# Performance work log

Hardware: AMD Instinct MI355X
Metric: run time of the kernel (lower is better)

## Reference

```python
import jax, jax.numpy as jnp
import numpy as np

# ---- static config (matches init_kwargs / input_specs) ----
MODEL_CONTEXT_LEN = 4096
BLOCK_SIZE = 16
NUM_Q_HEADS = 32
NUM_KV_HEADS = 8
HEAD_DIM = 128
ROPE_BASE = 10000.0
B = 8
NUM_PAST = 4613                                   # context_len - 1, same for all seqs
END_BNUM = NUM_PAST // BLOCK_SIZE                 # 288
REM = NUM_PAST % BLOCK_SIZE                       # 5
START_BNUM = (NUM_PAST - MODEL_CONTEXT_LEN) // BLOCK_SIZE + 2  # 34
CUR_POS = MODEL_CONTEXT_LEN - 1                   # 4095 (capped decode position)
BLOCKS_PER_SEQ = END_BNUM + 1                     # 289
NUM_BLOCKS = B * BLOCKS_PER_SEQ                   # 2312


def rope(pos, x):
    """NeoX-style rotary. pos: [T] int; x: [..., T, H, D]."""
    half = HEAD_DIM // 2
    inv = 1.0 / (ROPE_BASE ** (jnp.arange(half, dtype=jnp.float32) / half))
    freqs = pos.astype(jnp.float32)[:, None] * inv        # [T, half]
    cos = jnp.cos(freqs)[:, None, :]                      # [T, 1, half]
    sin = jnp.sin(freqs)[:, None, :]
    x1, x2 = jnp.split(x, 2, axis=-1)
    return jnp.concatenate([x1 * cos - x2 * sin, x2 * cos + x1 * sin], axis=-1)


def setup_inputs() -> dict:
    key = jax.random.key(0)
    ks = jax.random.split(key, 7)
    q = jax.random.normal(ks[0], (B, NUM_Q_HEADS * HEAD_DIM), jnp.float32)
    k = jax.random.normal(ks[1], (B, NUM_KV_HEADS * HEAD_DIM), jnp.float32)
    v = jax.random.normal(ks[2], (B, NUM_KV_HEADS * HEAD_DIM), jnp.float32)
    positions = jnp.full((B,), NUM_PAST, dtype=jnp.int32)
    context_lens = jnp.full((B,), NUM_PAST + 1, dtype=jnp.int32)
    # distinct physical blocks per sequence (paged layout)
    block_tables = jnp.arange(NUM_BLOCKS, dtype=jnp.int32).reshape(B, BLOCKS_PER_SEQ)
    # cache stores UN-rotated keys (module writes k_original); layout [nblk, bs, Hk, D]
    key_cache = jax.random.normal(ks[3], (NUM_BLOCKS, BLOCK_SIZE, NUM_KV_HEADS, HEAD_DIM), jnp.float32) * 0.5
    value_cache = jax.random.normal(ks[4], (NUM_BLOCKS, BLOCK_SIZE, NUM_KV_HEADS, HEAD_DIM), jnp.float32) * 0.5
    W_o = jax.random.normal(ks[5], (NUM_Q_HEADS * HEAD_DIM, NUM_Q_HEADS * HEAD_DIM), jnp.float32) * 0.02
    return {"q": q, "k": k, "v": v, "positions": positions, "context_lens": context_lens,
            "block_tables": block_tables, "key_cache": key_cache, "value_cache": value_cache, "W_o": W_o}


def reference(q, k, v, positions, context_lens, block_tables, key_cache, value_cache, W_o):
    # Decode path of StreamingAttentionSink, context > model_context_len:
    # gather sink block + sliding-window blocks, re-apply rotary at shifted
    # positions, attend with q/k roped at capped position, project output.
    # positions for re-roped past keys: sink tokens 0..bs-1, window tokens
    # 2*bs-1-rem .. model_context_len-2 (matches the torch code's pos arange).
    pos_sink = np.arange(BLOCK_SIZE)
    pos_win = np.arange(2 * BLOCK_SIZE - 1 - REM, MODEL_CONTEXT_LEN - 1)
    POS = jnp.asarray(np.concatenate([pos_sink, pos_win]), dtype=jnp.int32)  # [4085]

    qh = q.reshape(B, NUM_Q_HEADS, HEAD_DIM)
    kh = k.reshape(B, NUM_KV_HEADS, HEAD_DIM)
    vh = v.reshape(B, NUM_KV_HEADS, HEAD_DIM)

    # phys_bnums = [block_table[0]] + block_table[start:end]  -> [B, 255]
    phys = jnp.concatenate([block_tables[:, :1], block_tables[:, START_BNUM:END_BNUM]], axis=1)
    full_k = key_cache[phys].reshape(B, -1, NUM_KV_HEADS, HEAD_DIM)       # [B, 4080, Hk, D]
    rem_k = key_cache[block_tables[:, END_BNUM], :REM]                     # [B, 5, Hk, D]
    past_k = jnp.concatenate([full_k, rem_k], axis=1)                      # [B, 4085, Hk, D]
    full_v = value_cache[phys].reshape(B, -1, NUM_KV_HEADS, HEAD_DIM)
    rem_v = value_cache[block_tables[:, END_BNUM], :REM]
    past_v = jnp.concatenate([full_v, rem_v], axis=1)

    past_k = rope(POS, past_k)  # re-apply rotary to shifted sink/window keys

    cur = jnp.array([CUR_POS], dtype=jnp.int32)
    q_rot = rope(cur, qh[:, None, :, :])[:, 0]   # [B, H, D] at capped position
    k_rot = rope(cur, kh[:, None, :, :])[:, 0]   # [B, Hk, D]

    keys = jnp.concatenate([past_k, k_rot[:, None]], axis=1)   # [B, 4086, Hk, D]
    vals = jnp.concatenate([past_v, vh[:, None]], axis=1)

    # GQA attention (group = 4 q-heads per kv-head)
    G = NUM_Q_HEADS // NUM_KV_HEADS
    qg = q_rot.reshape(B, NUM_KV_HEADS, G, HEAD_DIM)
    scale = 1.0 / np.sqrt(HEAD_DIM).astype(np.float32)
    scores = jnp.einsum('bhgd,bthd->bhgt', qg, keys) * scale
    probs = jax.nn.softmax(scores, axis=-1)
    attn = jnp.einsum('bhgt,bthd->bhgd', probs, vals).reshape(B, NUM_Q_HEADS * HEAD_DIM)
    return attn @ W_o
```

## Files before the change

kernel.cpp:

```cpp
#include <hip/hip_runtime.h>
#include <math.h>

#define NB 8
#define NQH 32
#define NKVH 8
#define HD 128
#define GQ 4
#define T_TOT 4086
#define SPLITS 16
#define TCHUNK 256
#define TILE 32
#define PAD 132
#define BPS 289
#define LOG2_10K_OVER_64 0.2076205059304601f
#define SCALE 0.08838834764831843f

#define PART_ATTN_OFF 0
#define PART_ATTN_SZ  (64 * GQ * SPLITS * PAD)
#define ATTN_OFF      (PART_ATTN_OFF + PART_ATTN_SZ)
#define ATTN_SZ       (NB * 4096)
#define PART_GEMM_OFF (ATTN_OFF + ATTN_SZ)
#define PART_GEMM_SZ  (16 * 32768)

__global__ __launch_bounds__(256) void attn_partial_kernel(
    const float* __restrict__ q, const float* __restrict__ k, const float* __restrict__ v,
    const int* __restrict__ bt, const float* __restrict__ kc, const float* __restrict__ vc,
    float* __restrict__ part)
{
    __shared__ float kt[TILE][PAD];
    __shared__ float vt[TILE][PAD];
    __shared__ float qs[GQ][HD];
    __shared__ float sc[GQ][TILE];
    __shared__ float inv_s[64];
    __shared__ int   ptile[TILE];

    const int tid  = threadIdx.x;
    const int bh   = blockIdx.x;
    const int s    = blockIdx.y;
    const int b    = bh >> 3, h = bh & 7;
    const int lane = tid & 63, wave = tid >> 6;

    if (tid < 64) inv_s[tid] = exp2f(-(float)tid * LOG2_10K_OVER_64);
    __syncthreads();

    const float* qp = q + (size_t)b * (NQH * HD) + (size_t)h * (GQ * HD);
    for (int e = tid; e < GQ * HD; e += 256) {
        int g = e >> 7, d = e & 127, j = d & 63;
        float freq = 4095.0f * inv_s[j];
        float sn, cs; sincosf(freq, &sn, &cs);
        float x1 = qp[g * HD + j], x2 = qp[g * HD + j + 64];
        qs[g][d] = (d < 64) ? (x1 * cs - x2 * sn) : (x2 * cs + x1 * sn);
    }

    float m_run = -INFINITY, l_run = 0.0f, acc_lo = 0.0f, acc_hi = 0.0f;
    const int t0 = s * TCHUNK;
    const int* btb = bt + b * BPS;

    for (int tb = 0; tb < TCHUNK; tb += TILE) {
        __syncthreads();

        for (int e = tid; e < TILE * 32; e += 256) {
            int row = e >> 5, c4 = (e & 31) << 2;
            int tg = t0 + tb + row;
            if (tg <= T_TOT - 1) {
                const float *ksrc, *vsrc; int pos;
                if (tg == T_TOT - 1) {
                    ksrc = k + (size_t)(b * NKVH + h) * HD;
                    vsrc = v + (size_t)(b * NKVH + h) * HD;
                    pos = 4095;
                } else {
                    int bti, rr;
                    if (tg < 16)        { bti = 0;              rr = tg;        pos = tg;      }
                    else if (tg < 4080) { bti = 33 + (tg >> 4); rr = tg & 15;   pos = tg + 10; }
                    else                { bti = 288;            rr = tg - 4080; pos = tg + 10; }
                    int blk = btb[bti];
                    size_t off = (((size_t)blk * 16 + rr) * NKVH + h) * HD;
                    ksrc = kc + off; vsrc = vc + off;
                }
                float4 kk = *(const float4*)(ksrc + c4);
                float4 vv = *(const float4*)(vsrc + c4);
                *(float4*)&kt[row][c4] = kk;
                *(float4*)&vt[row][c4] = vv;
                if ((e & 31) == 0) ptile[row] = pos;
            } else {
                float4 z = {0.f, 0.f, 0.f, 0.f};
                *(float4*)&kt[row][c4] = z;
                *(float4*)&vt[row][c4] = z;
                if ((e & 31) == 0) ptile[row] = 0;
            }
        }
        __syncthreads();

        for (int e = tid; e < TILE * 64; e += 256) {
            int row = e >> 6, j = e & 63;
            float freq = (float)ptile[row] * inv_s[j];
            float sn, cs; sincosf(freq, &sn, &cs);
            float x1 = kt[row][j], x2 = kt[row][j + 64];
            kt[row][j]      = x1 * cs - x2 * sn;
            kt[row][j + 64] = x2 * cs + x1 * sn;
        }
        __syncthreads();

        if (tid < 128) {
            int t = tid & 31, g = tid >> 5;
            int tg = t0 + tb + t;
            float dot = 0.f;
            #pragma unroll
            for (int d4 = 0; d4 < 32; ++d4) {
                float4 kk = *(const float4*)&kt[t][d4 << 2];
                float4 qq = *(const float4*)&qs[g][d4 << 2];
                dot += kk.x * qq.x + kk.y * qq.y + kk.z * qq.z + kk.w * qq.w;
            }
            sc[g][t] = (tg <= T_TOT - 1) ? dot * SCALE : -INFINITY;
        }
        __syncthreads();

        {
            int g = wave;
            int tl = lane & 31;
            float sv = sc[g][tl];
            float mx = sv;
            #pragma unroll
            for (int off = 16; off; off >>= 1) mx = fmaxf(mx, __shfl_xor(mx, off));
            float m_new = fmaxf(m_run, mx);
            float alpha = expf(m_run - m_new);
            float p = expf(sv - m_new);
            float ps = p;
            #pragma unroll
            for (int off = 16; off; off >>= 1) ps += __shfl_xor(ps, off);
            l_run = l_run * alpha + ps;
            m_run = m_new;
            acc_lo *= alpha; acc_hi *= alpha;
            if (lane < 32) sc[g][tl] = p;
            #pragma unroll 8
            for (int t = 0; t < TILE; ++t) {
                float pv = sc[g][t];
                acc_lo += pv * vt[t][lane];
                acc_hi += pv * vt[t][lane + 64];
            }
        }
    }

    float* pp = part + ((size_t)(bh * GQ + wave) * SPLITS + s) * PAD;
    pp[lane] = acc_lo;
    pp[lane + 64] = acc_hi;
    if (lane == 0) { pp[128] = m_run; pp[129] = l_run; }
}

__global__ __launch_bounds__(256) void attn_reduce_kernel(
    const float* __restrict__ part, float* __restrict__ attn)
{
    int bh = blockIdx.x;
    int tid = threadIdx.x;
    int g = tid >> 6, lane = tid & 63;
    const float* pg = part + (size_t)(bh * GQ + g) * SPLITS * PAD;
    float mstar = -INFINITY;
    #pragma unroll
    for (int s = 0; s < SPLITS; ++s) mstar = fmaxf(mstar, pg[s * PAD + 128]);
    float accl = 0.f, acch = 0.f, l = 0.f;
    #pragma unroll
    for (int s = 0; s < SPLITS; ++s) {
        float w = expf(pg[s * PAD + 128] - mstar);
        l    += pg[s * PAD + 129] * w;
        accl += w * pg[s * PAD + lane];
        acch += w * pg[s * PAD + lane + 64];
    }
    int b = bh >> 3, h = bh & 7;
    float inv_l = 1.0f / l;
    size_t base = (size_t)b * 4096 + (size_t)(h * GQ + g) * 128;
    attn[base + lane]      = accl * inv_l;
    attn[base + lane + 64] = acch * inv_l;
}

__global__ __launch_bounds__(256) void gemm_partial_kernel(
    const float* __restrict__ attn, const float* __restrict__ Wo,
    float* __restrict__ part)
{
    __shared__ float a_s[NB][256];
    int tid = threadIdx.x;
    int jt = blockIdx.x & 15, is = blockIdx.x >> 4;
    int i0 = is * 256;
    int c  = jt * 256 + tid;
    for (int e = tid; e < NB * 256; e += 256) {
        int bb = e >> 8, i = e & 255;
        a_s[bb][i] = attn[(size_t)bb * 4096 + i0 + i];
    }
    __syncthreads();
    float acc[NB] = {0.f, 0.f, 0.f, 0.f, 0.f, 0.f, 0.f, 0.f};
    #pragma unroll 4
    for (int i = 0; i < 256; ++i) {
        float w = Wo[(size_t)(i0 + i) * 4096 + c];
        #pragma unroll
        for (int bb = 0; bb < NB; ++bb) acc[bb] += a_s[bb][i] * w;
    }
    for (int bb = 0; bb < NB; ++bb)
        part[(size_t)is * 32768 + (size_t)bb * 4096 + c] = acc[bb];
}

__global__ __launch_bounds__(256) void gemm_reduce_kernel(
    const float* __restrict__ part, float* __restrict__ out)
{
    int idx = blockIdx.x * 256 + threadIdx.x;
    float4 sum = {0.f, 0.f, 0.f, 0.f};
    #pragma unroll
    for (int s = 0; s < 16; ++s) {
        float4 p = *(const float4*)(part + (size_t)s * 32768 + (size_t)idx * 4);
        sum.x += p.x; sum.y += p.y; sum.z += p.z; sum.w += p.w;
    }
    *(float4*)(out + (size_t)idx * 4) = sum;
}

extern "C" void kernel_launch(void* const* d_in, const int* in_sizes, int n_in,
                              void* d_out, int out_size, void* d_ws, size_t ws_size,
                              hipStream_t stream) {
    const float* q  = (const float*)d_in[0];
    const float* k  = (const float*)d_in[1];
    const float* v  = (const float*)d_in[2];
    const int*   bt = (const int*)d_in[5];
    const float* kc = (const float*)d_in[6];
    const float* vc = (const float*)d_in[7];
    const float* Wo = (const float*)d_in[8];
    float* out = (float*)d_out;
    float* ws  = (float*)d_ws;

    float* part_attn = ws + PART_ATTN_OFF;
    float* attn      = ws + ATTN_OFF;
    float* part_gemm = ws + PART_GEMM_OFF;

    attn_partial_kernel<<<dim3(64, SPLITS), 256, 0, stream>>>(q, k, v, bt, kc, vc, part_attn);
    attn_reduce_kernel<<<64, 256, 0, stream>>>(part_attn, attn);
    gemm_partial_kernel<<<256, 256, 0, stream>>>(attn, Wo, part_gemm);
    gemm_reduce_kernel<<<32, 256, 0, stream>>>(part_gemm, out);
}
```

Before: 397.0 us.

## Precompute RoPE cos/sin table, fuse key rotation into load, split GEMM over more blocks

Adds a kernel that precomputes a 4096x128 cos/sin table in workspace, so the attention kernel no longer calls sincosf per key element. Key rotation is now done in registers as the key is loaded, which removes a shared-memory pass and one barrier per tile. The output GEMM grid grows from 256 to 1024 blocks, each covering 64 columns with a 4-way wave split over the reduction dimension and a shared-memory reduction, to raise parallelism. The cost is an extra launch plus table writes and reads, and the gemm partials now reuse the table's workspace region.

```diff
diff --git a/kernel.cpp b/kernel.cpp
--- a/kernel.cpp
+++ b/kernel.cpp
@@ -15,24 +15,33 @@
 #define LOG2_10K_OVER_64 0.2076205059304601f
 #define SCALE 0.08838834764831843f
 
-#define PART_ATTN_OFF 0
+#define TAB_OFF       0
+#define TAB_SZ        (4096 * 128)
+#define PART_GEMM_OFF 0
+#define PART_ATTN_OFF TAB_SZ
 #define PART_ATTN_SZ  (64 * GQ * SPLITS * PAD)
 #define ATTN_OFF      (PART_ATTN_OFF + PART_ATTN_SZ)
-#define ATTN_SZ       (NB * 4096)
-#define PART_GEMM_OFF (ATTN_OFF + ATTN_SZ)
-#define PART_GEMM_SZ  (16 * 32768)
+
+__global__ __launch_bounds__(256) void rope_table_kernel(float* __restrict__ tab)
+{
+    int idx = blockIdx.x * 256 + threadIdx.x;
+    int pos = idx >> 6, j = idx & 63;
+    float inv = exp2f(-(float)j * LOG2_10K_OVER_64);
+    float freq = (float)pos * inv;
+    float sn, cs; sincosf(freq, &sn, &cs);
+    tab[pos * 128 + j]      = cs;
+    tab[pos * 128 + 64 + j] = sn;
+}
 
 __global__ __launch_bounds__(256) void attn_partial_kernel(
     const float* __restrict__ q, const float* __restrict__ k, const float* __restrict__ v,
     const int* __restrict__ bt, const float* __restrict__ kc, const float* __restrict__ vc,
-    float* __restrict__ part)
+    const float* __restrict__ tab, float* __restrict__ part)
 {
     __shared__ float kt[TILE][PAD];
     __shared__ float vt[TILE][PAD];
     __shared__ float qs[GQ][HD];
     __shared__ float sc[GQ][TILE];
-    __shared__ float inv_s[64];
-    __shared__ int   ptile[TILE];
 
     const int tid  = threadIdx.x;
     const int bh   = blockIdx.x;
@@ -40,14 +49,11 @@
     const int b    = bh >> 3, h = bh & 7;
     const int lane = tid & 63, wave = tid >> 6;
 
-    if (tid < 64) inv_s[tid] = exp2f(-(float)tid * LOG2_10K_OVER_64);
-    __syncthreads();
-
     const float* qp = q + (size_t)b * (NQH * HD) + (size_t)h * (GQ * HD);
+    const float* trow = tab + 4095 * 128;
     for (int e = tid; e < GQ * HD; e += 256) {
         int g = e >> 7, d = e & 127, j = d & 63;
-        float freq = 4095.0f * inv_s[j];
-        float sn, cs; sincosf(freq, &sn, &cs);
+        float cs = trow[j], sn = trow[64 + j];
         float x1 = qp[g * HD + j], x2 = qp[g * HD + j + 64];
         qs[g][d] = (d < 64) ? (x1 * cs - x2 * sn) : (x2 * cs + x1 * sn);
     }
@@ -59,14 +65,13 @@
     for (int tb = 0; tb < TCHUNK; tb += TILE) {
         __syncthreads();
 
-        for (int e = tid; e < TILE * 32; e += 256) {
-            int row = e >> 5, c4 = (e & 31) << 2;
+        for (int e = tid; e < TILE * 16; e += 256) {
+            int row = e >> 4, c4 = (e & 15) << 2;
             int tg = t0 + tb + row;
             if (tg <= T_TOT - 1) {
-                const float *ksrc, *vsrc; int pos;
+                const float* ksrc; int pos;
                 if (tg == T_TOT - 1) {
                     ksrc = k + (size_t)(b * NKVH + h) * HD;
-                    vsrc = v + (size_t)(b * NKVH + h) * HD;
                     pos = 4095;
                 } else {
                     int bti, rr;
@@ -74,30 +79,45 @@
                     else if (tg < 4080) { bti = 33 + (tg >> 4); rr = tg & 15;   pos = tg + 10; }
                     else                { bti = 288;            rr = tg - 4080; pos = tg + 10; }
                     int blk = btb[bti];
-                    size_t off = (((size_t)blk * 16 + rr) * NKVH + h) * HD;
-                    ksrc = kc + off; vsrc = vc + off;
+                    ksrc = kc + (((size_t)blk * 16 + rr) * NKVH + h) * HD;
                 }
-                float4 kk = *(const float4*)(ksrc + c4);
-                float4 vv = *(const float4*)(vsrc + c4);
-                *(float4*)&kt[row][c4] = kk;
-                *(float4*)&vt[row][c4] = vv;
-                if ((e & 31) == 0) ptile[row] = pos;
+                float4 k1 = *(const float4*)(ksrc + c4);
+                float4 k2 = *(const float4*)(ksrc + 64 + c4);
+                float4 cs = *(const float4*)(tab + (size_t)pos * 128 + c4);
+                float4 sn = *(const float4*)(tab + (size_t)pos * 128 + 64 + c4);
+                float4 lo, hi;
+                lo.x = k1.x * cs.x - k2.x * sn.x;  hi.x = k2.x * cs.x + k1.x * sn.x;
+                lo.y = k1.y * cs.y - k2.y * sn.y;  hi.y = k2.y * cs.y + k1.y * sn.y;
+                lo.z = k1.z * cs.z - k2.z * sn.z;  hi.z = k2.z * cs.z + k1.z * sn.z;
+                lo.w = k1.w * cs.w - k2.w * sn.w;  hi.w = k2.w * cs.w + k1.w * sn.w;
+                *(float4*)&kt[row][c4]      = lo;
+                *(float4*)&kt[row][64 + c4] = hi;
             } else {
                 float4 z = {0.f, 0.f, 0.f, 0.f};
-                *(float4*)&kt[row][c4] = z;
+                *(float4*)&kt[row][c4]      = z;
+                *(float4*)&kt[row][64 + c4] = z;
+            }
+        }
+        for (int e = tid; e < TILE * 32; e += 256) {
+            int row = e >> 5, c4 = (e & 31) << 2;
+            int tg = t0 + tb + row;
+            if (tg <= T_TOT - 1) {
+                const float* vsrc;
+                if (tg == T_TOT - 1) {
+                    vsrc = v + (size_t)(b * NKVH + h) * HD;
+                } else {
+                    int bti, rr;
+                    if (tg < 16)        { bti = 0;              rr = tg;        }
+                    else if (tg < 4080) { bti = 33 + (tg >> 4); rr = tg & 15;   }
+                    else                { bti = 288;            rr = tg - 4080; }
+                    int blk = btb[bti];
+                    vsrc = vc + (((size_t)blk * 16 + rr) * NKVH + h) * HD;
+                }
+                *(float4*)&vt[row][c4] = *(const float4*)(vsrc + c4);
+            } else {
+                float4 z = {0.f, 0.f, 0.f, 0.f};
                 *(float4*)&vt[row][c4] = z;
-                if ((e & 31) == 0) ptile[row] = 0;
-            }
-        }
-        __syncthreads();
-
-        for (int e = tid; e < TILE * 64; e += 256) {
-            int row = e >> 6, j = e & 63;
-            float freq = (float)ptile[row] * inv_s[j];
-            float sn, cs; sincosf(freq, &sn, &cs);
-            float x1 = kt[row][j], x2 = kt[row][j + 64];
-            kt[row][j]      = x1 * cs - x2 * sn;
-            kt[row][j + 64] = x2 * cs + x1 * sn;
+            }
         }
         __syncthreads();
 
@@ -177,24 +197,35 @@
     float* __restrict__ part)
 {
     __shared__ float a_s[NB][256];
+    __shared__ float red[4][NB][64];
     int tid = threadIdx.x;
-    int jt = blockIdx.x & 15, is = blockIdx.x >> 4;
+    int lane = tid & 63, w = tid >> 6;
+    int jt = blockIdx.x;
+    int is = blockIdx.y;
     int i0 = is * 256;
-    int c  = jt * 256 + tid;
+    int c  = jt * 64 + lane;
     for (int e = tid; e < NB * 256; e += 256) {
         int bb = e >> 8, i = e & 255;
         a_s[bb][i] = attn[(size_t)bb * 4096 + i0 + i];
     }
     __syncthreads();
     float acc[NB] = {0.f, 0.f, 0.f, 0.f, 0.f, 0.f, 0.f, 0.f};
+    const float* wp = Wo + (size_t)(i0 + w * 64) * 4096 + c;
     #pragma unroll 4
-    for (int i = 0; i < 256; ++i) {
-        float w = Wo[(size_t)(i0 + i) * 4096 + c];
+    for (int ii = 0; ii < 64; ++ii) {
+        float wv = wp[(size_t)ii * 4096];
+        int i_loc = w * 64 + ii;
         #pragma unroll
-        for (int bb = 0; bb < NB; ++bb) acc[bb] += a_s[bb][i] * w;
-    }
-    for (int bb = 0; bb < NB; ++bb)
-        part[(size_t)is * 32768 + (size_t)bb * 4096 + c] = acc[bb];
+        for (int bb = 0; bb < NB; ++bb) acc[bb] += a_s[bb][i_loc] * wv;
+    }
+    #pragma unroll
+    for (int bb = 0; bb < NB; ++bb) red[w][bb][lane] = acc[bb];
+    __syncthreads();
+    for (int e = tid; e < NB * 64; e += 256) {
+        int bb = e >> 6, l = e & 63;
+        float sum = red[0][bb][l] + red[1][bb][l] + red[2][bb][l] + red[3][bb][l];
+        part[(size_t)is * 32768 + (size_t)bb * 4096 + jt * 64 + l] = sum;
+    }
 }
 
 __global__ __launch_bounds__(256) void gemm_reduce_kernel(
@@ -223,12 +254,14 @@
     float* out = (float*)d_out;
     float* ws  = (float*)d_ws;
 
+    float* tab       = ws + TAB_OFF;
     float* part_attn = ws + PART_ATTN_OFF;
     float* attn      = ws + ATTN_OFF;
     float* part_gemm = ws + PART_GEMM_OFF;
 
-    attn_partial_kernel<<<dim3(64, SPLITS), 256, 0, stream>>>(q, k, v, bt, kc, vc, part_attn);
+    rope_table_kernel<<<1024, 256, 0, stream>>>(tab);
+    attn_partial_kernel<<<dim3(64, SPLITS), 256, 0, stream>>>(q, k, v, bt, kc, vc, tab, part_attn);
     attn_reduce_kernel<<<64, 256, 0, stream>>>(part_attn, attn);
-    gemm_partial_kernel<<<256, 256, 0, stream>>>(attn, Wo, part_gemm);
+    gemm_partial_kernel<<<dim3(64, 16), 256, 0, stream>>>(attn, Wo, part_gemm);
     gemm_reduce_kernel<<<32, 256, 0, stream>>>(part_gemm, out);
 }
```

After: 380.9 us. 1.04x faster.
